# Optimization experiments

Hardware: AMD Instinct MI355X
Metric: run time of the kernel (lower is better)

Reference implementation:

```python
import jax, jax.numpy as jnp
import numpy as np

# dims per init_kwargs / input_specs
N, F_IN, H, C, L = 50000, 128, 128, 40, 4
E = 800000
ALPHA = 0.1   # args.beta -> self.alpha (initial-residual strength)
LAMDA = 0.5   # identity-mapping decay


def setup_inputs() -> dict:
    key = jax.random.key(0)
    ks = jax.random.split(key, 6)
    x = jax.random.normal(ks[0], (N, F_IN), jnp.float32)
    edge_index = jax.random.randint(ks[1], (2, E), 0, N, dtype=jnp.int32)
    s = 1.0 / np.sqrt(H)
    W_in = jax.random.uniform(ks[2], (F_IN, H), jnp.float32, -s, s)
    b_in = jnp.zeros((H,), jnp.float32)
    W_layers = jax.random.uniform(ks[3], (L, H, H), jnp.float32, -s, s)
    W_out = jax.random.uniform(ks[4], (H, C), jnp.float32, -s, s)
    b_out = jnp.zeros((C,), jnp.float32)
    return dict(x=x, edge_index=edge_index, W_in=W_in, b_in=b_in,
                W_layers=W_layers, W_out=W_out, b_out=b_out)


def _gcn_norm(edge_index, n):
    """Symmetric GCN normalization with added self-loops (gcn_norm)."""
    loops = jnp.arange(n, dtype=edge_index.dtype)
    row = jnp.concatenate([edge_index[0], loops])  # destination
    col = jnp.concatenate([edge_index[1], loops])  # source
    deg = jax.ops.segment_sum(jnp.ones(row.shape, jnp.float32), row, num_segments=n)
    dinv = jnp.where(deg > 0, jax.lax.rsqrt(jnp.maximum(deg, 1e-12)), 0.0)
    return row, col, dinv[row] * dinv[col]  # per-edge norm coefficient


def reference(x, edge_index, W_in, b_in, W_layers, W_out, b_out):
    n = x.shape[0]
    row, col, norm = _gcn_norm(edge_index, n)
    # input linear + relu (dropout is identity in eval / p=0)
    h = jax.nn.relu(x @ W_in + b_in)
    h0 = h  # _hidden[0], the initial residual
    # beta_i = log(lamda/(i+1) + 1)
    betas = jnp.log(LAMDA / jnp.arange(1, L + 1, dtype=jnp.float32) + 1.0)

    def layer(h, wb):
        W, beta = wb
        # sparse graph conv: gather-source, scale, scatter-add to dest  [E,H] msgs
        agg = jax.ops.segment_sum(h[col] * norm[:, None], row, num_segments=n)
        support = (1.0 - ALPHA) * agg + ALPHA * h0
        out = beta * (support @ W) + (1.0 - beta) * support  # ((1-b)I + bW)
        return jax.nn.relu(out), None

    h, _ = jax.lax.scan(layer, h, (W_layers, betas))
    return h @ W_out + b_out
```

## Files before the change

### kernel.cpp

```cpp
#include <hip/hip_runtime.h>
#include <hip/hip_bf16.h>
#include <hip/hip_fp16.h>
#include <math.h>

typedef short short8 __attribute__((ext_vector_type(8)));
typedef _Float16 half8 __attribute__((ext_vector_type(8)));
typedef float f32x4  __attribute__((ext_vector_type(4)));

__device__ __forceinline__ unsigned short f2h(float f) {
    return __half_as_ushort(__float2half(f));
}
__device__ __forceinline__ float h2f(unsigned short u) {
    return __half2float(__ushort_as_half(u));
}


__global__ void k_zero(uint4* __restrict__ p, int n16) {
    int i = blockIdx.x * 256 + threadIdx.x;
    if (i < n16) p[i] = make_uint4(0u, 0u, 0u, 0u);
}


__global__ void k_count(const int* __restrict__ dst, int* __restrict__ cnt,
                        unsigned short* __restrict__ rank, int E) {
    int e = blockIdx.x * 256 + threadIdx.x;
    if (e < E) rank[e] = (unsigned short)atomicAdd(&cnt[dst[e]], 1);
}

__global__ void k_scan_part(const int* __restrict__ cnt, int* __restrict__ offs,
                            int* __restrict__ parts, float* __restrict__ dinv, int n) {
    __shared__ int s[256];
    int i = blockIdx.x * 256 + threadIdx.x;
    int v = (i < n) ? cnt[i] : 0;
    s[threadIdx.x] = v;
    __syncthreads();
    #pragma unroll
    for (int d = 1; d < 256; d <<= 1) {
        int t = (threadIdx.x >= d) ? s[threadIdx.x - d] : 0;
        __syncthreads();
        s[threadIdx.x] += t;
        __syncthreads();
    }
    if (i < n) {
        offs[i] = s[threadIdx.x] - v;
        dinv[i] = rsqrtf((float)v + 1.0f);
    }
    if (threadIdx.x == 255) parts[blockIdx.x] = s[255];
}

__global__ void k_scan_tops(int* __restrict__ parts, int np) {
    __shared__ int s[256];
    int tid = threadIdx.x;
    int v = (tid < np) ? parts[tid] : 0;
    s[tid] = v;
    __syncthreads();
    #pragma unroll
    for (int d = 1; d < 256; d <<= 1) {
        int t = (tid >= d) ? s[tid - d] : 0;
        __syncthreads();
        s[tid] += t;
        __syncthreads();
    }
    if (tid < np) parts[tid] = s[tid] - v;
}

__global__ void k_scan_add(int* __restrict__ offs, const int* __restrict__ parts,
                           int n, int e_total) {
    int i = blockIdx.x * 256 + threadIdx.x;
    if (i < n) offs[i] += parts[blockIdx.x];
    if (blockIdx.x == 0 && threadIdx.x == 0) offs[n] = e_total;
}

__global__ void k_scatter(const int* __restrict__ dst, const int* __restrict__ src,
                          const unsigned short* __restrict__ rank,
                          const int* __restrict__ offs,
                          const float* __restrict__ dinv,
                          unsigned* __restrict__ csr, int E) {
    int e = blockIdx.x * 256 + threadIdx.x;
    if (e < E) {
        int d = dst[e], s = src[e];
        float w = 0.9f * dinv[d] * dinv[s];
        csr[offs[d] + (int)rank[e]] = ((unsigned)f2h(w) << 16) | (unsigned)s;
    }
}


__global__ void k_wprep(const float* __restrict__ Wl, const float* __restrict__ Win,
                        const float* __restrict__ Wout,
                        unsigned short* __restrict__ wt,
                        unsigned short* __restrict__ wint,
                        unsigned short* __restrict__ wot, int C) {
    int m = blockIdx.x;
    if (m < 4) {
        for (int i = threadIdx.x; i < 16384; i += 256) {
            int n = i >> 7, k = i & 127;
            wt[m * 16384 + n * 128 + k] = f2h(Wl[m * 16384 + k * 128 + n]);
        }
    } else if (m == 4) {
        for (int i = threadIdx.x; i < 16384; i += 256) {
            int n = i >> 7, k = i & 127;
            wint[n * 128 + k] = f2h(Win[k * 128 + n]);
        }
    } else {
        for (int i = threadIdx.x; i < 48 * 128; i += 256) {
            int n = i >> 7, k = i & 127;
            wot[n * 128 + k] = (n < C) ? f2h(Wout[k * C + n]) : (unsigned short)0;
        }
    }
}


__global__ __launch_bounds__(256)
void k_spmm(const int* __restrict__ offs, const unsigned* __restrict__ csr,
            const unsigned short* __restrict__ hb,
            const unsigned short* __restrict__ h0b,
            const float* __restrict__ dinv,
            unsigned short* __restrict__ supb, int n, int E) {
    int node = blockIdx.x * 8 + (threadIdx.x >> 5);
    if (node >= n) return;
    int l32 = threadIdx.x & 31;
    float di = dinv[node];
    float ws = 0.9f * di * di;
    uint2 sv = *(const uint2*)&hb [((size_t)node << 7) + (l32 << 2)];
    uint2 rv = *(const uint2*)&h0b[((size_t)node << 7) + (l32 << 2)];
    float ax = ws * h2f((unsigned short)(sv.x & 0xffffu)) + 0.1f * h2f((unsigned short)(rv.x & 0xffffu));
    float ay = ws * h2f((unsigned short)(sv.x >> 16))     + 0.1f * h2f((unsigned short)(rv.x >> 16));
    float az = ws * h2f((unsigned short)(sv.y & 0xffffu)) + 0.1f * h2f((unsigned short)(rv.y & 0xffffu));
    float aw = ws * h2f((unsigned short)(sv.y >> 16))     + 0.1f * h2f((unsigned short)(rv.y >> 16));
    int e = offs[node], end = offs[node + 1];
    while (e < end) {
        int nb = end - e;
        if (nb > 32) nb = 32;
        unsigned ce = csr[min(e + l32, E - 1)];
        int i = 0;
        for (; i + 16 <= nb; i += 16) {
            uint2 g[16]; float wv[16];
            #pragma unroll
            for (int j = 0; j < 16; ++j) {
                unsigned u = __shfl(ce, i + j, 32);
                wv[j] = h2f((unsigned short)(u >> 16));
                g[j] = *(const uint2*)&hb[((size_t)(u & 0xffffu) << 7) + (l32 << 2)];
            }
            #pragma unroll
            for (int j = 0; j < 16; ++j) {
                ax += wv[j] * h2f((unsigned short)(g[j].x & 0xffffu));
                ay += wv[j] * h2f((unsigned short)(g[j].x >> 16));
                az += wv[j] * h2f((unsigned short)(g[j].y & 0xffffu));
                aw += wv[j] * h2f((unsigned short)(g[j].y >> 16));
            }
        }
        for (; i + 8 <= nb; i += 8) {
            uint2 g[8]; float wv[8];
            #pragma unroll
            for (int j = 0; j < 8; ++j) {
                unsigned u = __shfl(ce, i + j, 32);
                wv[j] = h2f((unsigned short)(u >> 16));
                g[j] = *(const uint2*)&hb[((size_t)(u & 0xffffu) << 7) + (l32 << 2)];
            }
            #pragma unroll
            for (int j = 0; j < 8; ++j) {
                ax += wv[j] * h2f((unsigned short)(g[j].x & 0xffffu));
                ay += wv[j] * h2f((unsigned short)(g[j].x >> 16));
                az += wv[j] * h2f((unsigned short)(g[j].y & 0xffffu));
                aw += wv[j] * h2f((unsigned short)(g[j].y >> 16));
            }
        }
        for (; i + 4 <= nb; i += 4) {
            uint2 g[4]; float wv[4];
            #pragma unroll
            for (int j = 0; j < 4; ++j) {
                unsigned u = __shfl(ce, i + j, 32);
                wv[j] = h2f((unsigned short)(u >> 16));
                g[j] = *(const uint2*)&hb[((size_t)(u & 0xffffu) << 7) + (l32 << 2)];
            }
            #pragma unroll
            for (int j = 0; j < 4; ++j) {
                ax += wv[j] * h2f((unsigned short)(g[j].x & 0xffffu));
                ay += wv[j] * h2f((unsigned short)(g[j].x >> 16));
                az += wv[j] * h2f((unsigned short)(g[j].y & 0xffffu));
                aw += wv[j] * h2f((unsigned short)(g[j].y >> 16));
            }
        }
        for (; i + 2 <= nb; i += 2) {
            uint2 g[2]; float wv[2];
            #pragma unroll
            for (int j = 0; j < 2; ++j) {
                unsigned u = __shfl(ce, i + j, 32);
                wv[j] = h2f((unsigned short)(u >> 16));
                g[j] = *(const uint2*)&hb[((size_t)(u & 0xffffu) << 7) + (l32 << 2)];
            }
            #pragma unroll
            for (int j = 0; j < 2; ++j) {
                ax += wv[j] * h2f((unsigned short)(g[j].x & 0xffffu));
                ay += wv[j] * h2f((unsigned short)(g[j].x >> 16));
                az += wv[j] * h2f((unsigned short)(g[j].y & 0xffffu));
                aw += wv[j] * h2f((unsigned short)(g[j].y >> 16));
            }
        }
        for (; i < nb; ++i) {
            unsigned u = __shfl(ce, i, 32);
            float w = h2f((unsigned short)(u >> 16));
            uint2 g = *(const uint2*)&hb[((size_t)(u & 0xffffu) << 7) + (l32 << 2)];
            ax += w * h2f((unsigned short)(g.x & 0xffffu));
            ay += w * h2f((unsigned short)(g.x >> 16));
            az += w * h2f((unsigned short)(g.y & 0xffffu));
            aw += w * h2f((unsigned short)(g.y >> 16));
        }
        e += nb;
    }
    uint2 o;
    o.x = (unsigned)f2h(ax) | ((unsigned)f2h(ay) << 16);
    o.y = (unsigned)f2h(az) | ((unsigned)f2h(aw) << 16);
    *(uint2*)&supb[((size_t)node << 7) + (l32 << 2)] = o;
}


__global__ __launch_bounds__(256)
void gemm_in(const float* __restrict__ inA,
             const unsigned short* __restrict__ Bh,
             const float* __restrict__ bias,
             unsigned short* __restrict__ hb,
             unsigned short* __restrict__ h0b, int M) {
    extern __shared__ char lds[];
    char* Ah = lds;
    char* Wh = Ah + 16384;

    const int tid  = threadIdx.x;
    const int row0 = blockIdx.x * 64;

    for (int c = tid; c < 1024; c += 256) {
        int row = c >> 4, k8 = c & 15;
        int grow = row0 + row;
        short8 hv = {0,0,0,0,0,0,0,0};
        if (grow < M) {
            const float* s = &inA[(size_t)grow * 128 + k8 * 8];
            float4 f0 = *(const float4*)s;
            float4 f1 = *(const float4*)(s + 4);
            float ff[8] = {f0.x, f0.y, f0.z, f0.w, f1.x, f1.y, f1.z, f1.w};
            #pragma unroll
            for (int j = 0; j < 8; ++j) hv[j] = (short)f2h(ff[j]);
        }
        *(short8*)(Ah + row * 256 + ((k8 ^ (row & 7)) << 4)) = hv;
    }
    for (int c = tid; c < 2048; c += 256) {
        int n = c >> 4, k8 = c & 15;
        *(short8*)(Wh + n * 256 + ((k8 ^ (n & 7)) << 4)) = *(const short8*)&Bh[n * 128 + k8 * 8];
    }
    __syncthreads();

    const int lane = tid & 63;
    const int w    = tid >> 6;
    const int lr   = lane & 15;
    const int lg   = lane >> 4;

    f32x4 acc[4][2];
    #pragma unroll
    for (int m = 0; m < 4; ++m)
        #pragma unroll
        for (int n2 = 0; n2 < 2; ++n2) acc[m][n2] = (f32x4){0.f, 0.f, 0.f, 0.f};

    #pragma unroll
    for (int kk = 0; kk < 4; ++kk) {
        int k8 = kk * 4 + lg;
        half8 a[4], b[2];
        #pragma unroll
        for (int m = 0; m < 4; ++m) {
            int row = m * 16 + lr;
            a[m] = *(const half8*)(Ah + row * 256 + ((k8 ^ (row & 7)) << 4));
        }
        #pragma unroll
        for (int n2 = 0; n2 < 2; ++n2) {
            int n = (w * 2 + n2) * 16 + lr;
            b[n2] = *(const half8*)(Wh + n * 256 + ((k8 ^ (n & 7)) << 4));
        }
        #pragma unroll
        for (int m = 0; m < 4; ++m)
            #pragma unroll
            for (int n2 = 0; n2 < 2; ++n2)
                acc[m][n2] = __builtin_amdgcn_mfma_f32_16x16x32_f16(a[m], b[n2], acc[m][n2], 0, 0, 0);
    }

    #pragma unroll
    for (int m = 0; m < 4; ++m) {
        #pragma unroll
        for (int n2 = 0; n2 < 2; ++n2) {
            int col = (w * 2 + n2) * 16 + lr;
            #pragma unroll
            for (int r = 0; r < 4; ++r) {
                int row = row0 + m * 16 + lg * 4 + r;
                if (row < M) {
                    float o = fmaxf(acc[m][n2][r] + bias[col], 0.f);
                    unsigned short ob = f2h(o);
                    hb [(size_t)row * 128 + col] = ob;
                    h0b[(size_t)row * 128 + col] = ob;
                }
            }
        }
    }
}


__global__ __launch_bounds__(256)
void gemm_layer(const unsigned short* __restrict__ supb,
                const unsigned short* __restrict__ Bh,
                float beta, float gamma,
                unsigned short* __restrict__ outh, int M) {
    extern __shared__ char lds[];
    char* Ah = lds;
    char* Wh = Ah + 16384;

    const int tid  = threadIdx.x;
    const int row0 = blockIdx.x * 64;

    for (int c = tid; c < 1024; c += 256) {
        int row = c >> 4, k8 = c & 15;
        int grow = row0 + row;
        short8 hv = {0,0,0,0,0,0,0,0};
        if (grow < M) hv = *(const short8*)&supb[(size_t)grow * 128 + k8 * 8];
        *(short8*)(Ah + row * 256 + ((k8 ^ (row & 7)) << 4)) = hv;
    }
    for (int c = tid; c < 2048; c += 256) {
        int n = c >> 4, k8 = c & 15;
        *(short8*)(Wh + n * 256 + ((k8 ^ (n & 7)) << 4)) = *(const short8*)&Bh[n * 128 + k8 * 8];
    }
    __syncthreads();

    const int lane = tid & 63;
    const int w    = tid >> 6;
    const int lr   = lane & 15;
    const int lg   = lane >> 4;

    f32x4 acc[4][2];
    #pragma unroll
    for (int m = 0; m < 4; ++m)
        #pragma unroll
        for (int n2 = 0; n2 < 2; ++n2) acc[m][n2] = (f32x4){0.f, 0.f, 0.f, 0.f};

    #pragma unroll
    for (int kk = 0; kk < 4; ++kk) {
        int k8 = kk * 4 + lg;
        half8 a[4], b[2];
        #pragma unroll
        for (int m = 0; m < 4; ++m) {
            int row = m * 16 + lr;
            a[m] = *(const half8*)(Ah + row * 256 + ((k8 ^ (row & 7)) << 4));
        }
        #pragma unroll
        for (int n2 = 0; n2 < 2; ++n2) {
            int n = (w * 2 + n2) * 16 + lr;
            b[n2] = *(const half8*)(Wh + n * 256 + ((k8 ^ (n & 7)) << 4));
        }
        #pragma unroll
        for (int m = 0; m < 4; ++m)
            #pragma unroll
            for (int n2 = 0; n2 < 2; ++n2)
                acc[m][n2] = __builtin_amdgcn_mfma_f32_16x16x32_f16(a[m], b[n2], acc[m][n2], 0, 0, 0);
    }

    #pragma unroll
    for (int m = 0; m < 4; ++m) {
        #pragma unroll
        for (int n2 = 0; n2 < 2; ++n2) {
            int col = (w * 2 + n2) * 16 + lr;
            int k8c = col >> 3;
            int ebc = (col & 7) * 2;
            #pragma unroll
            for (int r = 0; r < 4; ++r) {
                int rl  = m * 16 + lg * 4 + r;
                int row = row0 + rl;
                if (row < M) {
                    unsigned short rb = *(const unsigned short*)
                        (Ah + rl * 256 + ((k8c ^ (rl & 7)) << 4) + ebc);
                    float o = beta * acc[m][n2][r] + gamma * h2f(rb);
                    o = fmaxf(o, 0.f);
                    outh[(size_t)row * 128 + col] = f2h(o);
                }
            }
        }
    }
}


__global__ __launch_bounds__(256)
void k_out(const unsigned short* __restrict__ hb,
           const unsigned short* __restrict__ Wot,
           const float* __restrict__ bias,
           float* __restrict__ out, int M, int C) {
    extern __shared__ char lds[];
    char* Ah = lds;
    char* Wh = Ah + 16384;

    const int tid  = threadIdx.x;
    const int row0 = blockIdx.x * 64;

    for (int c = tid; c < 1024; c += 256) {
        int row = c >> 4, k8 = c & 15;
        int grow = row0 + row;
        short8 hv = {0,0,0,0,0,0,0,0};
        if (grow < M) hv = *(const short8*)&hb[(size_t)grow * 128 + k8 * 8];
        *(short8*)(Ah + row * 256 + ((k8 ^ (row & 7)) << 4)) = hv;
    }
    for (int c = tid; c < 768; c += 256) {
        int n = c >> 4, k8 = c & 15;
        *(short8*)(Wh + n * 256 + ((k8 ^ (n & 7)) << 4)) = *(const short8*)&Wot[n * 128 + k8 * 8];
    }
    __syncthreads();

    const int lane = tid & 63;
    const int w    = tid >> 6;
    const int lr   = lane & 15;
    const int lg   = lane >> 4;

    f32x4 acc[3];
    #pragma unroll
    for (int n2 = 0; n2 < 3; ++n2) acc[n2] = (f32x4){0.f, 0.f, 0.f, 0.f};

    #pragma unroll
    for (int kk = 0; kk < 4; ++kk) {
        int k8 = kk * 4 + lg;
        int row = w * 16 + lr;
        half8 a = *(const half8*)(Ah + row * 256 + ((k8 ^ (row & 7)) << 4));
        #pragma unroll
        for (int n2 = 0; n2 < 3; ++n2) {
            int n = n2 * 16 + lr;
            half8 b = *(const half8*)(Wh + n * 256 + ((k8 ^ (n & 7)) << 4));
            acc[n2] = __builtin_amdgcn_mfma_f32_16x16x32_f16(a, b, acc[n2], 0, 0, 0);
        }
    }

    #pragma unroll
    for (int n2 = 0; n2 < 3; ++n2) {
        int col = n2 * 16 + lr;
        if (col < C) {
            float bb = bias[col];
            #pragma unroll
            for (int r = 0; r < 4; ++r) {
                int row = row0 + w * 16 + lg * 4 + r;
                if (row < M) out[(size_t)row * C + col] = acc[n2][r] + bb;
            }
        }
    }
}


extern "C" void kernel_launch(void* const* d_in, const int* in_sizes, int n_in,
                              void* d_out, int out_size, void* d_ws, size_t ws_size,
                              hipStream_t stream) {
    const float* x        = (const float*)d_in[0];
    const int*   ei       = (const int*)d_in[1];
    const float* W_in     = (const float*)d_in[2];
    const float* b_in     = (const float*)d_in[3];
    const float* W_layers = (const float*)d_in[4];
    const float* W_out    = (const float*)d_in[5];
    const float* b_out    = (const float*)d_in[6];
    float* out = (float*)d_out;

    const int H = 128;
    const int N = in_sizes[0] / H;
    const int E = in_sizes[1] / 2;
    const int L = in_sizes[4] / (H * H);
    const int C = in_sizes[5] / H;

    char* p = (char*)d_ws;
    auto alloc = [&](size_t bytes) {
        char* r = p;
        p += (bytes + 255) & ~(size_t)255;
        return r;
    };
    int*      cnt   = (int*)alloc((size_t)N * 4);
    int*      offs  = (int*)alloc((size_t)(N + 1) * 4);
    int*      parts = (int*)alloc(256 * 4);
    unsigned* csr   = (unsigned*)alloc((size_t)E * 4);
    unsigned short* rank = (unsigned short*)alloc((size_t)E * 2);
    float*    dinv  = (float*)alloc((size_t)N * 4);
    unsigned short* hb   = (unsigned short*)alloc((size_t)N * H * 2);
    unsigned short* h0b  = (unsigned short*)alloc((size_t)N * H * 2);
    unsigned short* supb = (unsigned short*)alloc((size_t)N * H * 2);
    unsigned short* wt   = (unsigned short*)alloc((size_t)L * H * H * 2);
    unsigned short* wint = (unsigned short*)alloc((size_t)H * H * 2);
    unsigned short* wot  = (unsigned short*)alloc((size_t)48 * H * 2);
    (void)ws_size;

    const int* ei0 = ei;
    const int* ei1 = ei + E;

    const int nblkN = (N + 255) / 256;
    const int nblkE = (E + 255) / 256;
    const int n16   = (N + 3) / 4;

    k_wprep<<<6, 256, 0, stream>>>(W_layers, W_in, W_out, wt, wint, wot, C);

    k_zero<<<(n16 + 255) / 256, 256, 0, stream>>>((uint4*)cnt, n16);
    k_count<<<nblkE, 256, 0, stream>>>(ei0, cnt, rank, E);
    k_scan_part<<<nblkN, 256, 0, stream>>>(cnt, offs, parts, dinv, N);
    k_scan_tops<<<1, 256, 0, stream>>>(parts, nblkN);
    k_scan_add<<<nblkN, 256, 0, stream>>>(offs, parts, N, E);
    k_scatter<<<nblkE, 256, 0, stream>>>(ei0, ei1, rank, offs, dinv, csr, E);

    gemm_in<<<(N + 63) / 64, 256, 48 * 1024, stream>>>(x, wint, b_in, hb, h0b, N);

    for (int l = 0; l < L; ++l) {
        float beta = logf(0.5f / (float)(l + 1) + 1.0f);
        k_spmm<<<(N + 7) / 8, 256, 0, stream>>>(offs, csr, hb, h0b, dinv, supb, N, E);
        gemm_layer<<<(N + 63) / 64, 256, 48 * 1024, stream>>>(
            supb, wt + (size_t)l * H * H, beta, 1.0f - beta, hb, N);
    }

    k_out<<<(N + 63) / 64, 256, 28 * 1024, stream>>>(hb, wot, b_out, out, N, C);
}
```

Before: 294.6 us.

## Fuse SpMM aggregation into layer GEMM and fold output projection into last layer

Each layer's sparse aggregation now runs inside the GEMM kernel. Every block gathers its 64 rows of support directly into LDS, so the supb intermediate no longer has to be written to and read back from global memory, and one launch per layer is removed. The hidden state ping-pongs between two buffers because gather reads and row writes would otherwise race across blocks. The final layer also performs the output projection from LDS, which removes the separate k_out kernel. The trade-off is that the gather phase now runs at 64-row block granularity and shares occupancy with the GEMM's 48KB of LDS, which may reduce memory-latency hiding for the irregular gathers.

```diff
diff --git a/kernel.cpp b/kernel.cpp
--- a/kernel.cpp
+++ b/kernel.cpp
@@ -111,111 +111,6 @@
 
 
 __global__ __launch_bounds__(256)
-void k_spmm(const int* __restrict__ offs, const unsigned* __restrict__ csr,
-            const unsigned short* __restrict__ hb,
-            const unsigned short* __restrict__ h0b,
-            const float* __restrict__ dinv,
-            unsigned short* __restrict__ supb, int n, int E) {
-    int node = blockIdx.x * 8 + (threadIdx.x >> 5);
-    if (node >= n) return;
-    int l32 = threadIdx.x & 31;
-    float di = dinv[node];
-    float ws = 0.9f * di * di;
-    uint2 sv = *(const uint2*)&hb [((size_t)node << 7) + (l32 << 2)];
-    uint2 rv = *(const uint2*)&h0b[((size_t)node << 7) + (l32 << 2)];
-    float ax = ws * h2f((unsigned short)(sv.x & 0xffffu)) + 0.1f * h2f((unsigned short)(rv.x & 0xffffu));
-    float ay = ws * h2f((unsigned short)(sv.x >> 16))     + 0.1f * h2f((unsigned short)(rv.x >> 16));
-    float az = ws * h2f((unsigned short)(sv.y & 0xffffu)) + 0.1f * h2f((unsigned short)(rv.y & 0xffffu));
-    float aw = ws * h2f((unsigned short)(sv.y >> 16))     + 0.1f * h2f((unsigned short)(rv.y >> 16));
-    int e = offs[node], end = offs[node + 1];
-    while (e < end) {
-        int nb = end - e;
-        if (nb > 32) nb = 32;
-        unsigned ce = csr[min(e + l32, E - 1)];
-        int i = 0;
-        for (; i + 16 <= nb; i += 16) {
-            uint2 g[16]; float wv[16];
-            #pragma unroll
-            for (int j = 0; j < 16; ++j) {
-                unsigned u = __shfl(ce, i + j, 32);
-                wv[j] = h2f((unsigned short)(u >> 16));
-                g[j] = *(const uint2*)&hb[((size_t)(u & 0xffffu) << 7) + (l32 << 2)];
-            }
-            #pragma unroll
-            for (int j = 0; j < 16; ++j) {
-                ax += wv[j] * h2f((unsigned short)(g[j].x & 0xffffu));
-                ay += wv[j] * h2f((unsigned short)(g[j].x >> 16));
-                az += wv[j] * h2f((unsigned short)(g[j].y & 0xffffu));
-                aw += wv[j] * h2f((unsigned short)(g[j].y >> 16));
-            }
-        }
-        for (; i + 8 <= nb; i += 8) {
-            uint2 g[8]; float wv[8];
-            #pragma unroll
-            for (int j = 0; j < 8; ++j) {
-                unsigned u = __shfl(ce, i + j, 32);
-                wv[j] = h2f((unsigned short)(u >> 16));
-                g[j] = *(const uint2*)&hb[((size_t)(u & 0xffffu) << 7) + (l32 << 2)];
-            }
-            #pragma unroll
-            for (int j = 0; j < 8; ++j) {
-                ax += wv[j] * h2f((unsigned short)(g[j].x & 0xffffu));
-                ay += wv[j] * h2f((unsigned short)(g[j].x >> 16));
-                az += wv[j] * h2f((unsigned short)(g[j].y & 0xffffu));
-                aw += wv[j] * h2f((unsigned short)(g[j].y >> 16));
-            }
-        }
-        for (; i + 4 <= nb; i += 4) {
-            uint2 g[4]; float wv[4];
-            #pragma unroll
-            for (int j = 0; j < 4; ++j) {
-                unsigned u = __shfl(ce, i + j, 32);
-                wv[j] = h2f((unsigned short)(u >> 16));
-                g[j] = *(const uint2*)&hb[((size_t)(u & 0xffffu) << 7) + (l32 << 2)];
-            }
-            #pragma unroll
-            for (int j = 0; j < 4; ++j) {
-                ax += wv[j] * h2f((unsigned short)(g[j].x & 0xffffu));
-                ay += wv[j] * h2f((unsigned short)(g[j].x >> 16));
-                az += wv[j] * h2f((unsigned short)(g[j].y & 0xffffu));
-                aw += wv[j] * h2f((unsigned short)(g[j].y >> 16));
-            }
-        }
-        for (; i + 2 <= nb; i += 2) {
-            uint2 g[2]; float wv[2];
-            #pragma unroll
-            for (int j = 0; j < 2; ++j) {
-                unsigned u = __shfl(ce, i + j, 32);
-                wv[j] = h2f((unsigned short)(u >> 16));
-                g[j] = *(const uint2*)&hb[((size_t)(u & 0xffffu) << 7) + (l32 << 2)];
-            }
-            #pragma unroll
-            for (int j = 0; j < 2; ++j) {
-                ax += wv[j] * h2f((unsigned short)(g[j].x & 0xffffu));
-                ay += wv[j] * h2f((unsigned short)(g[j].x >> 16));
-                az += wv[j] * h2f((unsigned short)(g[j].y & 0xffffu));
-                aw += wv[j] * h2f((unsigned short)(g[j].y >> 16));
-            }
-        }
-        for (; i < nb; ++i) {
-            unsigned u = __shfl(ce, i, 32);
-            float w = h2f((unsigned short)(u >> 16));
-            uint2 g = *(const uint2*)&hb[((size_t)(u & 0xffffu) << 7) + (l32 << 2)];
-            ax += w * h2f((unsigned short)(g.x & 0xffffu));
-            ay += w * h2f((unsigned short)(g.x >> 16));
-            az += w * h2f((unsigned short)(g.y & 0xffffu));
-            aw += w * h2f((unsigned short)(g.y >> 16));
-        }
-        e += nb;
-    }
-    uint2 o;
-    o.x = (unsigned)f2h(ax) | ((unsigned)f2h(ay) << 16);
-    o.y = (unsigned)f2h(az) | ((unsigned)f2h(aw) << 16);
-    *(uint2*)&supb[((size_t)node << 7) + (l32 << 2)] = o;
-}
-
-
-__global__ __launch_bounds__(256)
 void gemm_in(const float* __restrict__ inA,
              const unsigned short* __restrict__ Bh,
              const float* __restrict__ bias,
@@ -300,11 +195,19 @@
 }
 
 
+template<int LAST>
 __global__ __launch_bounds__(256)
-void gemm_layer(const unsigned short* __restrict__ supb,
-                const unsigned short* __restrict__ Bh,
-                float beta, float gamma,
-                unsigned short* __restrict__ outh, int M) {
+void k_layer(const int* __restrict__ offs, const unsigned* __restrict__ csr,
+             const unsigned short* __restrict__ hin,
+             const unsigned short* __restrict__ h0b,
+             const float* __restrict__ dinv,
+             const unsigned short* __restrict__ Bh,
+             const unsigned short* __restrict__ Wot,
+             const float* __restrict__ obias,
+             float beta, float gamma,
+             unsigned short* __restrict__ hout,
+             float* __restrict__ outf,
+             int M, int C, int E) {
     extern __shared__ char lds[];
     char* Ah = lds;
     char* Wh = Ah + 16384;
@@ -312,16 +215,113 @@
     const int tid  = threadIdx.x;
     const int row0 = blockIdx.x * 64;
 
-    for (int c = tid; c < 1024; c += 256) {
-        int row = c >> 4, k8 = c & 15;
-        int grow = row0 + row;
-        short8 hv = {0,0,0,0,0,0,0,0};
-        if (grow < M) hv = *(const short8*)&supb[(size_t)grow * 128 + k8 * 8];
-        *(short8*)(Ah + row * 256 + ((k8 ^ (row & 7)) << 4)) = hv;
-    }
     for (int c = tid; c < 2048; c += 256) {
         int n = c >> 4, k8 = c & 15;
         *(short8*)(Wh + n * 256 + ((k8 ^ (n & 7)) << 4)) = *(const short8*)&Bh[n * 128 + k8 * 8];
+    }
+
+    const int hw  = tid >> 5;
+    const int l32 = tid & 31;
+    for (int it = 0; it < 8; ++it) {
+        int li   = hw * 8 + it;
+        int node = row0 + li;
+        float ax = 0.f, ay = 0.f, az = 0.f, aw = 0.f;
+        if (node < M) {
+            float di = dinv[node];
+            float ws = 0.9f * di * di;
+            uint2 sv = *(const uint2*)&hin[((size_t)node << 7) + (l32 << 2)];
+            uint2 rv = *(const uint2*)&h0b[((size_t)node << 7) + (l32 << 2)];
+            ax = ws * h2f((unsigned short)(sv.x & 0xffffu)) + 0.1f * h2f((unsigned short)(rv.x & 0xffffu));
+            ay = ws * h2f((unsigned short)(sv.x >> 16))     + 0.1f * h2f((unsigned short)(rv.x >> 16));
+            az = ws * h2f((unsigned short)(sv.y & 0xffffu)) + 0.1f * h2f((unsigned short)(rv.y & 0xffffu));
+            aw = ws * h2f((unsigned short)(sv.y >> 16))     + 0.1f * h2f((unsigned short)(rv.y >> 16));
+            int e = offs[node], end = offs[node + 1];
+            while (e < end) {
+                int nb = end - e;
+                if (nb > 32) nb = 32;
+                unsigned ce = csr[min(e + l32, E - 1)];
+                int i = 0;
+                for (; i + 16 <= nb; i += 16) {
+                    uint2 g[16]; float wv[16];
+                    #pragma unroll
+                    for (int j = 0; j < 16; ++j) {
+                        unsigned u = __shfl(ce, i + j, 32);
+                        wv[j] = h2f((unsigned short)(u >> 16));
+                        g[j] = *(const uint2*)&hin[((size_t)(u & 0xffffu) << 7) + (l32 << 2)];
+                    }
+                    #pragma unroll
+                    for (int j = 0; j < 16; ++j) {
+                        ax += wv[j] * h2f((unsigned short)(g[j].x & 0xffffu));
+                        ay += wv[j] * h2f((unsigned short)(g[j].x >> 16));
+                        az += wv[j] * h2f((unsigned short)(g[j].y & 0xffffu));
+                        aw += wv[j] * h2f((unsigned short)(g[j].y >> 16));
+                    }
+                }
+                for (; i + 8 <= nb; i += 8) {
+                    uint2 g[8]; float wv[8];
+                    #pragma unroll
+                    for (int j = 0; j < 8; ++j) {
+                        unsigned u = __shfl(ce, i + j, 32);
+                        wv[j] = h2f((unsigned short)(u >> 16));
+                        g[j] = *(const uint2*)&hin[((size_t)(u & 0xffffu) << 7) + (l32 << 2)];
+                    }
+                    #pragma unroll
+                    for (int j = 0; j < 8; ++j) {
+                        ax += wv[j] * h2f((unsigned short)(g[j].x & 0xffffu));
+                        ay += wv[j] * h2f((unsigned short)(g[j].x >> 16));
+                        az += wv[j] * h2f((unsigned short)(g[j].y & 0xffffu));
+                        aw += wv[j] * h2f((unsigned short)(g[j].y >> 16));
+                    }
+                }
+                for (; i + 4 <= nb; i += 4) {
+                    uint2 g[4]; float wv[4];
+                    #pragma unroll
+                    for (int j = 0; j < 4; ++j) {
+                        unsigned u = __shfl(ce, i + j, 32);
+                        wv[j] = h2f((unsigned short)(u >> 16));
+                        g[j] = *(const uint2*)&hin[((size_t)(u & 0xffffu) << 7) + (l32 << 2)];
+                    }
+                    #pragma unroll
+                    for (int j = 0; j < 4; ++j) {
+                        ax += wv[j] * h2f((unsigned short)(g[j].x & 0xffffu));
+                        ay += wv[j] * h2f((unsigned short)(g[j].x >> 16));
+                        az += wv[j] * h2f((unsigned short)(g[j].y & 0xffffu));
+                        aw += wv[j] * h2f((unsigned short)(g[j].y >> 16));
+                    }
+                }
+                for (; i + 2 <= nb; i += 2) {
+                    uint2 g[2]; float wv[2];
+                    #pragma unroll
+                    for (int j = 0; j < 2; ++j) {
+                        unsigned u = __shfl(ce, i + j, 32);
+                        wv[j] = h2f((unsigned short)(u >> 16));
+                        g[j] = *(const uint2*)&hin[((size_t)(u & 0xffffu) << 7) + (l32 << 2)];
+                    }
+                    #pragma unroll
+                    for (int j = 0; j < 2; ++j) {
+                        ax += wv[j] * h2f((unsigned short)(g[j].x & 0xffffu));
+                        ay += wv[j] * h2f((unsigned short)(g[j].x >> 16));
+                        az += wv[j] * h2f((unsigned short)(g[j].y & 0xffffu));
+                        aw += wv[j] * h2f((unsigned short)(g[j].y >> 16));
+                    }
+                }
+                for (; i < nb; ++i) {
+                    unsigned u = __shfl(ce, i, 32);
+                    float w = h2f((unsigned short)(u >> 16));
+                    uint2 g = *(const uint2*)&hin[((size_t)(u & 0xffffu) << 7) + (l32 << 2)];
+                    ax += w * h2f((unsigned short)(g.x & 0xffffu));
+                    ay += w * h2f((unsigned short)(g.x >> 16));
+                    az += w * h2f((unsigned short)(g.y & 0xffffu));
+                    aw += w * h2f((unsigned short)(g.y >> 16));
+                }
+                e += nb;
+            }
+        }
+        unsigned plo = (unsigned)f2h(ax) | ((unsigned)f2h(ay) << 16);
+        unsigned phi = (unsigned)f2h(az) | ((unsigned)f2h(aw) << 16);
+        int k8  = l32 >> 1;
+        int off = li * 256 + ((k8 ^ (li & 7)) << 4) + (l32 & 1) * 8;
+        *(uint2*)(Ah + off) = make_uint2(plo, phi);
     }
     __syncthreads();
 
@@ -368,75 +368,55 @@
             for (int r = 0; r < 4; ++r) {
                 int rl  = m * 16 + lg * 4 + r;
                 int row = row0 + rl;
-                if (row < M) {
-                    unsigned short rb = *(const unsigned short*)
-                        (Ah + rl * 256 + ((k8c ^ (rl & 7)) << 4) + ebc);
-                    float o = beta * acc[m][n2][r] + gamma * h2f(rb);
-                    o = fmaxf(o, 0.f);
-                    outh[(size_t)row * 128 + col] = f2h(o);
+                unsigned short rb = *(const unsigned short*)
+                    (Ah + rl * 256 + ((k8c ^ (rl & 7)) << 4) + ebc);
+                float o = beta * acc[m][n2][r] + gamma * h2f(rb);
+                o = fmaxf(o, 0.f);
+                if (!LAST) {
+                    if (row < M) hout[(size_t)row * 128 + col] = f2h(o);
+                } else {
+                    *(unsigned short*)
+                        (Ah + rl * 256 + ((k8c ^ (rl & 7)) << 4) + ebc) = f2h(o);
                 }
             }
         }
     }
-}
-
-
-__global__ __launch_bounds__(256)
-void k_out(const unsigned short* __restrict__ hb,
-           const unsigned short* __restrict__ Wot,
-           const float* __restrict__ bias,
-           float* __restrict__ out, int M, int C) {
-    extern __shared__ char lds[];
-    char* Ah = lds;
-    char* Wh = Ah + 16384;
-
-    const int tid  = threadIdx.x;
-    const int row0 = blockIdx.x * 64;
-
-    for (int c = tid; c < 1024; c += 256) {
-        int row = c >> 4, k8 = c & 15;
-        int grow = row0 + row;
-        short8 hv = {0,0,0,0,0,0,0,0};
-        if (grow < M) hv = *(const short8*)&hb[(size_t)grow * 128 + k8 * 8];
-        *(short8*)(Ah + row * 256 + ((k8 ^ (row & 7)) << 4)) = hv;
-    }
-    for (int c = tid; c < 768; c += 256) {
-        int n = c >> 4, k8 = c & 15;
-        *(short8*)(Wh + n * 256 + ((k8 ^ (n & 7)) << 4)) = *(const short8*)&Wot[n * 128 + k8 * 8];
-    }
-    __syncthreads();
-
-    const int lane = tid & 63;
-    const int w    = tid >> 6;
-    const int lr   = lane & 15;
-    const int lg   = lane >> 4;
-
-    f32x4 acc[3];
-    #pragma unroll
-    for (int n2 = 0; n2 < 3; ++n2) acc[n2] = (f32x4){0.f, 0.f, 0.f, 0.f};
-
-    #pragma unroll
-    for (int kk = 0; kk < 4; ++kk) {
-        int k8 = kk * 4 + lg;
-        int row = w * 16 + lr;
-        half8 a = *(const half8*)(Ah + row * 256 + ((k8 ^ (row & 7)) << 4));
+
+    if (LAST) {
+        __syncthreads();
+        for (int c = tid; c < 768; c += 256) {
+            int n = c >> 4, k8 = c & 15;
+            *(short8*)(Wh + n * 256 + ((k8 ^ (n & 7)) << 4)) = *(const short8*)&Wot[n * 128 + k8 * 8];
+        }
+        __syncthreads();
+
+        f32x4 oacc[3];
+        #pragma unroll
+        for (int n2 = 0; n2 < 3; ++n2) oacc[n2] = (f32x4){0.f, 0.f, 0.f, 0.f};
+
+        #pragma unroll
+        for (int kk = 0; kk < 4; ++kk) {
+            int k8 = kk * 4 + lg;
+            int row = w * 16 + lr;
+            half8 a = *(const half8*)(Ah + row * 256 + ((k8 ^ (row & 7)) << 4));
+            #pragma unroll
+            for (int n2 = 0; n2 < 3; ++n2) {
+                int n = n2 * 16 + lr;
+                half8 b = *(const half8*)(Wh + n * 256 + ((k8 ^ (n & 7)) << 4));
+                oacc[n2] = __builtin_amdgcn_mfma_f32_16x16x32_f16(a, b, oacc[n2], 0, 0, 0);
+            }
+        }
+
         #pragma unroll
         for (int n2 = 0; n2 < 3; ++n2) {
-            int n = n2 * 16 + lr;
-            half8 b = *(const half8*)(Wh + n * 256 + ((k8 ^ (n & 7)) << 4));
-            acc[n2] = __builtin_amdgcn_mfma_f32_16x16x32_f16(a, b, acc[n2], 0, 0, 0);
-        }
-    }
-
-    #pragma unroll
-    for (int n2 = 0; n2 < 3; ++n2) {
-        int col = n2 * 16 + lr;
-        if (col < C) {
-            float bb = bias[col];
-            #pragma unroll
-            for (int r = 0; r < 4; ++r) {
-                int row = row0 + w * 16 + lg * 4 + r;
-                if (row < M) out[(size_t)row * C + col] = acc[n2][r] + bb;
+            int col = n2 * 16 + lr;
+            if (col < C) {
+                float bb = obias[col];
+                #pragma unroll
+                for (int r = 0; r < 4; ++r) {
+                    int row = row0 + w * 16 + lg * 4 + r;
+                    if (row < M) outf[(size_t)row * C + col] = oacc[n2][r] + bb;
+                }
             }
         }
     }
@@ -473,9 +453,9 @@
     unsigned* csr   = (unsigned*)alloc((size_t)E * 4);
     unsigned short* rank = (unsigned short*)alloc((size_t)E * 2);
     float*    dinv  = (float*)alloc((size_t)N * 4);
-    unsigned short* hb   = (unsigned short*)alloc((size_t)N * H * 2);
+    unsigned short* hb0  = (unsigned short*)alloc((size_t)N * H * 2);
+    unsigned short* hb1  = (unsigned short*)alloc((size_t)N * H * 2);
     unsigned short* h0b  = (unsigned short*)alloc((size_t)N * H * 2);
-    unsigned short* supb = (unsigned short*)alloc((size_t)N * H * 2);
     unsigned short* wt   = (unsigned short*)alloc((size_t)L * H * H * 2);
     unsigned short* wint = (unsigned short*)alloc((size_t)H * H * 2);
     unsigned short* wot  = (unsigned short*)alloc((size_t)48 * H * 2);
@@ -497,14 +477,21 @@
     k_scan_add<<<nblkN, 256, 0, stream>>>(offs, parts, N, E);
     k_scatter<<<nblkE, 256, 0, stream>>>(ei0, ei1, rank, offs, dinv, csr, E);
 
-    gemm_in<<<(N + 63) / 64, 256, 48 * 1024, stream>>>(x, wint, b_in, hb, h0b, N);
-
+    gemm_in<<<(N + 63) / 64, 256, 48 * 1024, stream>>>(x, wint, b_in, hb0, h0b, N);
+
+    const int gblk = (N + 63) / 64;
+    unsigned short* bufs[2] = {hb0, hb1};
     for (int l = 0; l < L; ++l) {
         float beta = logf(0.5f / (float)(l + 1) + 1.0f);
-        k_spmm<<<(N + 7) / 8, 256, 0, stream>>>(offs, csr, hb, h0b, dinv, supb, N, E);
-        gemm_layer<<<(N + 63) / 64, 256, 48 * 1024, stream>>>(
-            supb, wt + (size_t)l * H * H, beta, 1.0f - beta, hb, N);
-    }
-
-    k_out<<<(N + 63) / 64, 256, 28 * 1024, stream>>>(hb, wot, b_out, out, N, C);
-}
+        unsigned short* hin  = bufs[l & 1];
+        unsigned short* houtb = bufs[(l + 1) & 1];
+        if (l < L - 1)
+            k_layer<0><<<gblk, 256, 48 * 1024, stream>>>(
+                offs, csr, hin, h0b, dinv, wt + (size_t)l * H * H,
+                nullptr, nullptr, beta, 1.0f - beta, houtb, nullptr, N, C, E);
+        else
+            k_layer<1><<<gblk, 256, 48 * 1024, stream>>>(
+                offs, csr, hin, h0b, dinv, wt + (size_t)l * H * H,
+                wot, b_out, beta, 1.0f - beta, nullptr, out, N, C, E);
+    }
+}
```

New measurement: 343.8 us. 16.7% more time.
